# Performance work log

Measured on AMD Instinct MI355X. Metric: run time of the kernel, lower is better.

Reference implementation:

```python
import jax, jax.numpy as jnp
import numpy as np

NEGATIVE_RATIO = 3.0


def setup_inputs() -> dict:
    key = jax.random.key(0)
    k1, k2, k3, k4, k5 = jax.random.split(key, 5)
    B, N, C = 64, 8732, 81  # batch, num_priors (SSD300), num_classes (COCO)
    pred_conf = jax.random.normal(k1, (B, N, C), dtype=jnp.float32)
    pred_loc = jax.random.normal(k2, (B, N, 4), dtype=jnp.float32)
    labels = jax.random.randint(k3, (B, N), 1, C)
    is_pos = jax.random.uniform(k4, (B, N)) < 0.03
    labels = jnp.where(is_pos, labels, 0)
    labels = labels.at[:, 0].set(1)  # guarantee >=1 positive per image
    gt_conf = jax.nn.one_hot(labels, C, dtype=jnp.float32)
    pos = (labels > 0)[..., None].astype(jnp.float32)
    gt_loc = jax.random.normal(k5, (B, N, 4), dtype=jnp.float32) * pos
    return {"pred_conf": pred_conf, "pred_loc": pred_loc,
            "gt_conf": gt_conf, "gt_loc": gt_loc}


def reference(pred_conf, pred_loc, gt_conf, gt_loc):
    B, N, _ = pred_conf.shape
    # ----- conf loss: cross entropy against one-hot gt -----
    conf_loss = -(jax.nn.log_softmax(pred_conf, axis=-1) * gt_conf).sum(-1)  # [B, N]
    pos_mask = gt_conf[:, :, 0] == 0  # non-background priors
    num_pos = pos_mask.sum(-1).astype(pred_conf.dtype)  # [B]
    pos_conf_loss = jnp.where(pos_mask, conf_loss, 0.0).sum(-1)  # [B]
    # ----- hard negative mining: keep losses strictly above k-th largest negative loss -----
    num_neg = num_pos * NEGATIVE_RATIO  # [B], float
    neg_loss = jnp.where(pos_mask, 0.0, conf_loss)  # zero out positives
    sorted_desc = -jnp.sort(-neg_loss, axis=-1)  # descending per row
    k = jnp.clip(num_neg.astype(jnp.int32), 0, N - 1)  # [B]
    thresh = jnp.take_along_axis(sorted_desc, k[:, None], axis=-1)  # [B, 1]
    neg_mask = neg_loss > thresh  # only true on negatives (pos entries are 0)
    neg_conf_loss = jnp.where(neg_mask, conf_loss, 0.0).sum(-1)  # [B]
    conf_total = pos_conf_loss / num_pos + neg_conf_loss / num_neg  # [B]
    # ----- loc loss: smooth L1 on priors with nonzero gt_loc -----
    loc_mask = gt_loc != 0  # [B, N, 4]
    num_pos_loc = jnp.any(loc_mask, axis=-1).sum(-1).astype(pred_loc.dtype)  # [B]
    diff = jnp.abs(pred_loc - gt_loc)
    smooth_l1 = jnp.where(diff < 1.0, 0.5 * diff * diff, diff - 0.5)
    loc_total = jnp.where(loc_mask, smooth_l1, 0.0).sum((-1, -2)) / num_pos_loc  # [B]
    return (conf_total + loc_total).mean()
```

## Files before the change

### kernel.cpp

```cpp
#include <hip/hip_runtime.h>
#include <math.h>

#define BB 64
#define NN 8732
#define CC 81
#define TR 64
#define TPB 4
#define CBX ((NN + TR * TPB - 1) / (TR * TPB))
#define LBX 5

__global__ void init_kernel(unsigned* acc, float* out) {
    int i = threadIdx.x;
    if (i < 4 * BB) acc[i] = 0u;
    if (i == 0) out[0] = 0.f;
}

__device__ __forceinline__ float4 ld4g(const float* __restrict__ p, size_t gf, size_t TOTF) {
    if (gf + 4 <= TOTF) return *(const float4*)(p + gf);
    float4 r; float* rp = (float*)&r;
    #pragma unroll
    for (int c = 0; c < 4; ++c) rp[c] = (gf + c < TOTF) ? p[gf + c] : 0.f;
    return r;
}

__global__ __launch_bounds__(256) void fused_kernel(
        const float* __restrict__ pred_conf,
        const float* __restrict__ gt_conf,
        const float* __restrict__ pred_loc,
        const float* __restrict__ gt_loc,
        float* __restrict__ neg_loss,
        int* __restrict__ num_pos,
        float* __restrict__ pos_sum,
        float* __restrict__ loc_cnt,
        float* __restrict__ loc_sum) {
    const int b   = blockIdx.y;
    const int tid = threadIdx.x;

    if (blockIdx.x >= CBX) {
        const int lb = blockIdx.x - CBX;
        const float4* pl = (const float4*)pred_loc;
        const float4* gl = (const float4*)gt_loc;
        float sum = 0.f, cnt = 0.f;
        #pragma unroll
        for (int j = 0; j < 8; ++j) {
            int n = lb * 2048 + j * 256 + tid;
            if (n < NN) {
                size_t idx = (size_t)b * NN + n;
                float4 p = pl[idx];
                float4 g = gl[idx];
                bool any = false;
                float pv[4] = {p.x, p.y, p.z, p.w};
                float gv[4] = {g.x, g.y, g.z, g.w};
                #pragma unroll
                for (int c = 0; c < 4; ++c) {
                    if (gv[c] != 0.f) {
                        any = true;
                        float d = fabsf(pv[c] - gv[c]);
                        sum += (d < 1.f) ? 0.5f * d * d : d - 0.5f;
                    }
                }
                if (any) cnt += 1.f;
            }
        }
        for (int o = 32; o; o >>= 1) {
            sum += __shfl_down(sum, o, 64);
            cnt += __shfl_down(cnt, o, 64);
        }
        __shared__ float ls_sum, ls_cnt;
        if (tid == 0) { ls_sum = 0.f; ls_cnt = 0.f; }
        __syncthreads();
        if ((tid & 63) == 0) { atomicAdd(&ls_sum, sum); atomicAdd(&ls_cnt, cnt); }
        __syncthreads();
        if (tid == 0) { atomicAdd(&loc_sum[b], ls_sum); atomicAdd(&loc_cnt[b], ls_cnt); }
        return;
    }

    __shared__ float lbuf[TR * CC + 8];
    __shared__ int   s_cnt;
    __shared__ float s_sum;
    float4* l4 = (float4*)lbuf;

    const size_t TOTF = (size_t)BB * NN * CC;
    const int tile0 = blockIdx.x * TPB;
    const int r = tid >> 2;
    const int h = tid & 3;

    if (tid == 0) { s_cnt = 0; s_sum = 0.f; }

    float4 rv[6];
    float  gt0p;
    int rowBn = tile0 * TR;
    int nrn   = min(TR, NN - rowBn);
    size_t a0n; int shn, t4n;
    {
        size_t seg = ((size_t)b * NN + rowBn) * CC;
        a0n = seg & ~(size_t)3; shn = (int)(seg - a0n);
        t4n = (shn + nrn * CC + 3) >> 2;
    }
    #pragma unroll
    for (int j = 0; j < 6; ++j) {
        int i = tid + 256 * j;
        if (i < t4n) rv[j] = ld4g(pred_conf, a0n + 4 * (size_t)i, TOTF);
    }
    gt0p = (r < nrn) ? gt_conf[((size_t)b * NN + rowBn + r) * CC] : 1.f;

    for (int t = 0; t < TPB; ++t) {
        const int   c_rowB = rowBn, c_nr = nrn, c_sh = shn, c_t4 = t4n;
        const float c_gt0  = gt0p;
        if (c_rowB >= NN) break;

        __syncthreads();
        #pragma unroll
        for (int j = 0; j < 6; ++j) {
            int i = tid + 256 * j;
            if (i < c_t4) l4[i] = rv[j];
        }
        __syncthreads();

        const int nrowB = (tile0 + t + 1) * TR;
        if (t + 1 < TPB && nrowB < NN) {
            rowBn = nrowB; nrn = min(TR, NN - nrowB);
            size_t seg = ((size_t)b * NN + nrowB) * CC;
            a0n = seg & ~(size_t)3; shn = (int)(seg - a0n);
            t4n = (shn + nrn * CC + 3) >> 2;
            #pragma unroll
            for (int j = 0; j < 6; ++j) {
                int i = tid + 256 * j;
                if (i < t4n) rv[j] = ld4g(pred_conf, a0n + 4 * (size_t)i, TOTF);
            }
            gt0p = (r < nrn) ? gt_conf[((size_t)b * NN + rowBn + r) * CC] : 1.f;
        } else {
            rowBn = NN;
        }

        if (r < c_nr) {
            const int c0 = h * 20 + (h > 0 ? 1 : 0);
            const int nc = (h == 0) ? 21 : 20;
            const float* row = lbuf + c_sh + r * CC;
            const size_t gbase = ((size_t)b * NN + c_rowB + r) * CC;

            float v[21];
            #pragma unroll
            for (int j = 0; j < 21; ++j)
                v[j] = (j < nc) ? row[c0 + j] : -1e30f;

            float m = v[0];
            #pragma unroll
            for (int j = 1; j < 21; ++j) m = fmaxf(m, v[j]);
            m = fmaxf(m, __shfl_xor(m, 1, 64));
            m = fmaxf(m, __shfl_xor(m, 2, 64));

            float e = 0.f;
            #pragma unroll
            for (int j = 0; j < 21; ++j) e += __expf(v[j] - m);
            e += __shfl_xor(e, 1, 64);
            e += __shfl_xor(e, 2, 64);

            const bool pos = (c_gt0 == 0.f);
            float x_sel = v[0];
            if (pos) {
                float d = 0.f;
                #pragma unroll
                for (int j = 0; j < 21; ++j)
                    if (j < nc) d += gt_conf[gbase + c0 + j] * v[j];
                d += __shfl_xor(d, 1, 64);
                d += __shfl_xor(d, 2, 64);
                x_sel = d;
            }

            const float loss = m + __logf(e) - x_sel;
            if (h == 0) {
                neg_loss[(size_t)b * NN + c_rowB + r] = pos ? 0.f : loss;
                if (pos) { atomicAdd(&s_cnt, 1); atomicAdd(&s_sum, loss); }
            }
        }
    }

    __syncthreads();
    if (tid == 0 && s_cnt) {
        atomicAdd(&num_pos[b], s_cnt);
        atomicAdd(&pos_sum[b], s_sum);
    }
}

__global__ __launch_bounds__(256) void select_kernel(
        const float* __restrict__ neg_loss,
        const int*   __restrict__ num_pos,
        const float* __restrict__ pos_sum,
        const float* __restrict__ loc_cnt,
        const float* __restrict__ loc_sum,
        float* __restrict__ out) {
    const int b    = blockIdx.x;
    const int tid  = threadIdx.x;
    const int lane = tid & 63;
    __shared__ unsigned vals[NN];
    __shared__ unsigned hist[256];
    __shared__ unsigned sh_prefix, sh_r;
    __shared__ float    s_part[4];

    #pragma unroll 4
    for (int i = tid; i < NN; i += 256)
        vals[i] = __float_as_uint(neg_loss[(size_t)b * NN + i]);

    const int np = num_pos[b];
    const int k  = min(3 * np, NN - 1);
    if (tid == 0) { sh_prefix = 0u; sh_r = (unsigned)k; }
    __syncthreads();

    unsigned prefix_mask = 0u;
    for (int p = 3; p >= 0; --p) {
        const unsigned pref = sh_prefix;
        const unsigned r    = sh_r;
        hist[tid] = 0u;
        __syncthreads();

        for (int i0 = 0; i0 < NN; i0 += 256) {
            const int i = i0 + tid;
            const bool act = (i < NN) && ((vals[i] & prefix_mask) == pref);
            const unsigned v   = act ? vals[i] : 0u;
            const unsigned bin = (v >> (8 * p)) & 255u;
            unsigned long long mm = __ballot(act);
            #pragma unroll
            for (int bit = 0; bit < 8; ++bit) {
                unsigned long long s = __ballot(act && ((bin >> bit) & 1u));
                mm &= ((bin >> bit) & 1u) ? s : ~s;
            }
            if (act && ((mm & ((1ull << lane) - 1ull)) == 0ull))
                atomicAdd(&hist[bin], (unsigned)__popcll(mm));
        }
        __syncthreads();

        if (tid < 64) {
            const unsigned h0 = hist[4 * tid + 0];
            const unsigned h1 = hist[4 * tid + 1];
            const unsigned h2 = hist[4 * tid + 2];
            const unsigned h3 = hist[4 * tid + 3];
            unsigned T = h0 + h1 + h2 + h3;
            #pragma unroll
            for (int off = 1; off < 64; off <<= 1) {
                unsigned t2 = __shfl_down(T, off, 64);
                if (tid + off < 64) T += t2;
            }
            unsigned Tn = __shfl_down(T, 1, 64);
            if (tid == 63) Tn = 0u;
            const unsigned S4 = Tn, S3 = S4 + h3, S2 = S3 + h2, S1 = S2 + h1, S0 = S1 + h0;
            int bin = -1; unsigned Slo = 0u;
            if      (S1 <= r && r < S0) { bin = 4 * tid + 0; Slo = S1; }
            else if (S2 <= r && r < S1) { bin = 4 * tid + 1; Slo = S2; }
            else if (S3 <= r && r < S2) { bin = 4 * tid + 2; Slo = S3; }
            else if (S4 <= r && r < S3) { bin = 4 * tid + 3; Slo = S4; }
            if (bin >= 0) {
                sh_r = r - Slo;
                sh_prefix = pref | ((unsigned)bin << (8 * p));
            }
        }
        __syncthreads();
        prefix_mask |= 0xFFu << (8 * p);
    }

    const float thresh = __uint_as_float(sh_prefix);
    float s = 0.f;
    #pragma unroll 4
    for (int i = tid; i < NN; i += 256) {
        float v = __uint_as_float(vals[i]);
        if (v > thresh) s += v;
    }
    for (int o = 32; o; o >>= 1) s += __shfl_down(s, o, 64);
    if (lane == 0) s_part[tid >> 6] = s;
    __syncthreads();
    if (tid == 0) {
        float neg_sum = s_part[0] + s_part[1] + s_part[2] + s_part[3];
        float npf = (float)np;
        float res = pos_sum[b] / npf + neg_sum / (3.0f * npf) + loc_sum[b] / loc_cnt[b];
        atomicAdd(out, res * (1.0f / BB));
    }
}

extern "C" void kernel_launch(void* const* d_in, const int* in_sizes, int n_in,
                              void* d_out, int out_size, void* d_ws, size_t ws_size,
                              hipStream_t stream) {
    const float* pred_conf = (const float*)d_in[0];
    const float* pred_loc  = (const float*)d_in[1];
    const float* gt_conf   = (const float*)d_in[2];
    const float* gt_loc    = (const float*)d_in[3];

    float* neg      = (float*)d_ws;
    int*   num_pos  = (int*)(neg + (size_t)BB * NN);
    float* pos_sum  = (float*)(num_pos + BB);
    float* loc_cnt  = pos_sum + BB;
    float* loc_sum  = loc_cnt + BB;

    init_kernel<<<1, 256, 0, stream>>>((unsigned*)num_pos, (float*)d_out);

    dim3 fgrid(CBX + LBX, BB);
    fused_kernel<<<fgrid, 256, 0, stream>>>(pred_conf, gt_conf, pred_loc, gt_loc,
                                            neg, num_pos, pos_sum, loc_cnt, loc_sum);

    select_kernel<<<BB, 256, 0, stream>>>(neg, num_pos, pos_sum, loc_cnt, loc_sum,
                                          (float*)d_out);
}
```

Baseline: 414.4 us.

## Give each wave its own LDS tile and drop block-wide barriers in conf loss

Restructures the cross-entropy stage so each 64-lane wave stages and processes its own 16-row tile in a private LDS region, removing the block-level __syncthreads between staging and compute. Positive-count and positive-loss accumulation moves from shared-memory atomics to per-lane registers reduced with wave shuffles, and the loc path now issues per-wave global atomics instead of a shared reduction. The intent is to cut barrier stalls and shared atomic contention, at the cost of smaller per-load tiles and more global atomics.

Measured after the change: 420.5 us. About the same (+1.5%).

```diff
diff --git a/kernel.cpp b/kernel.cpp
--- a/kernel.cpp
+++ b/kernel.cpp
@@ -4,10 +4,13 @@
 #define BB 64
 #define NN 8732
 #define CC 81
-#define TR 64
-#define TPB 4
-#define CBX ((NN + TR * TPB - 1) / (TR * TPB))
+#define TR2 16
+#define WIT 4
+#define WROWS (TR2 * WIT)
+#define BROWS (WROWS * 4)
+#define CBX ((NN + BROWS - 1) / BROWS)
 #define LBX 5
+#define LSEG4 328
 
 __global__ void init_kernel(unsigned* acc, float* out) {
     int i = threadIdx.x;
@@ -66,78 +69,78 @@
             sum += __shfl_down(sum, o, 64);
             cnt += __shfl_down(cnt, o, 64);
         }
-        __shared__ float ls_sum, ls_cnt;
-        if (tid == 0) { ls_sum = 0.f; ls_cnt = 0.f; }
-        __syncthreads();
-        if ((tid & 63) == 0) { atomicAdd(&ls_sum, sum); atomicAdd(&ls_cnt, cnt); }
-        __syncthreads();
-        if (tid == 0) { atomicAdd(&loc_sum[b], ls_sum); atomicAdd(&loc_cnt[b], ls_cnt); }
+        if ((tid & 63) == 0) {
+            atomicAdd(&loc_sum[b], sum);
+            atomicAdd(&loc_cnt[b], cnt);
+        }
         return;
     }
 
-    __shared__ float lbuf[TR * CC + 8];
-    __shared__ int   s_cnt;
-    __shared__ float s_sum;
-    float4* l4 = (float4*)lbuf;
+    __shared__ float4 lbuf4[4][LSEG4];
 
     const size_t TOTF = (size_t)BB * NN * CC;
-    const int tile0 = blockIdx.x * TPB;
-    const int r = tid >> 2;
-    const int h = tid & 3;
-
-    if (tid == 0) { s_cnt = 0; s_sum = 0.f; }
+    const int wave = tid >> 6;
+    const int lane = tid & 63;
+    const int q    = lane >> 2;
+    const int h    = lane & 3;
+    float*  lws = (float*)lbuf4[wave];
+    float4* l4  = lbuf4[wave];
+
+    const int rowB0 = blockIdx.x * BROWS + wave * WROWS;
+
+    int   my_cnt = 0;
+    float my_sum = 0.f;
 
     float4 rv[6];
-    float  gt0p;
-    int rowBn = tile0 * TR;
-    int nrn   = min(TR, NN - rowBn);
-    size_t a0n; int shn, t4n;
-    {
-        size_t seg = ((size_t)b * NN + rowBn) * CC;
-        a0n = seg & ~(size_t)3; shn = (int)(seg - a0n);
-        t4n = (shn + nrn * CC + 3) >> 2;
-    }
-    #pragma unroll
-    for (int j = 0; j < 6; ++j) {
-        int i = tid + 256 * j;
-        if (i < t4n) rv[j] = ld4g(pred_conf, a0n + 4 * (size_t)i, TOTF);
-    }
-    gt0p = (r < nrn) ? gt_conf[((size_t)b * NN + rowBn + r) * CC] : 1.f;
-
-    for (int t = 0; t < TPB; ++t) {
-        const int   c_rowB = rowBn, c_nr = nrn, c_sh = shn, c_t4 = t4n;
-        const float c_gt0  = gt0p;
-        if (c_rowB >= NN) break;
-
-        __syncthreads();
+    float  gt0p = 1.f;
+    int curB  = rowB0;
+    int curNr = min(TR2, NN - curB);
+    int curSh = 0, curT4 = 0;
+    if (curNr > 0) {
+        size_t seg = ((size_t)b * NN + curB) * CC;
+        size_t a0  = seg & ~(size_t)3;
+        curSh = (int)(seg - a0);
+        curT4 = (curSh + curNr * CC + 3) >> 2;
         #pragma unroll
         for (int j = 0; j < 6; ++j) {
-            int i = tid + 256 * j;
+            int i = lane + 64 * j;
+            if (i < curT4) rv[j] = ld4g(pred_conf, a0 + 4 * (size_t)i, TOTF);
+        }
+        if (q < curNr) gt0p = gt_conf[((size_t)b * NN + curB + q) * CC];
+    }
+
+    for (int it = 0; it < WIT; ++it) {
+        const int   c_rowB = curB, c_nr = curNr, c_sh = curSh, c_t4 = curT4;
+        const float c_gt0  = gt0p;
+        if (c_nr <= 0) break;
+
+        #pragma unroll
+        for (int j = 0; j < 6; ++j) {
+            int i = lane + 64 * j;
             if (i < c_t4) l4[i] = rv[j];
         }
-        __syncthreads();
-
-        const int nrowB = (tile0 + t + 1) * TR;
-        if (t + 1 < TPB && nrowB < NN) {
-            rowBn = nrowB; nrn = min(TR, NN - nrowB);
-            size_t seg = ((size_t)b * NN + nrowB) * CC;
-            a0n = seg & ~(size_t)3; shn = (int)(seg - a0n);
-            t4n = (shn + nrn * CC + 3) >> 2;
+
+        const int nB  = rowB0 + (it + 1) * TR2;
+        const int nNr = (it + 1 < WIT) ? min(TR2, NN - nB) : 0;
+        if (nNr > 0) {
+            size_t seg = ((size_t)b * NN + nB) * CC;
+            size_t a0  = seg & ~(size_t)3;
+            curSh = (int)(seg - a0);
+            curT4 = (curSh + nNr * CC + 3) >> 2;
             #pragma unroll
             for (int j = 0; j < 6; ++j) {
-                int i = tid + 256 * j;
-                if (i < t4n) rv[j] = ld4g(pred_conf, a0n + 4 * (size_t)i, TOTF);
-            }
-            gt0p = (r < nrn) ? gt_conf[((size_t)b * NN + rowBn + r) * CC] : 1.f;
-        } else {
-            rowBn = NN;
-        }
-
-        if (r < c_nr) {
+                int i = lane + 64 * j;
+                if (i < curT4) rv[j] = ld4g(pred_conf, a0 + 4 * (size_t)i, TOTF);
+            }
+            gt0p = (q < nNr) ? gt_conf[((size_t)b * NN + nB + q) * CC] : 1.f;
+        }
+        curB = nB; curNr = nNr;
+
+        if (q < c_nr) {
             const int c0 = h * 20 + (h > 0 ? 1 : 0);
             const int nc = (h == 0) ? 21 : 20;
-            const float* row = lbuf + c_sh + r * CC;
-            const size_t gbase = ((size_t)b * NN + c_rowB + r) * CC;
+            const float* row = lws + c_sh + q * CC;
+            const size_t gbase = ((size_t)b * NN + c_rowB + q) * CC;
 
             float v[21];
             #pragma unroll
@@ -170,16 +173,20 @@
 
             const float loss = m + __logf(e) - x_sel;
             if (h == 0) {
-                neg_loss[(size_t)b * NN + c_rowB + r] = pos ? 0.f : loss;
-                if (pos) { atomicAdd(&s_cnt, 1); atomicAdd(&s_sum, loss); }
-            }
-        }
-    }
-
-    __syncthreads();
-    if (tid == 0 && s_cnt) {
-        atomicAdd(&num_pos[b], s_cnt);
-        atomicAdd(&pos_sum[b], s_sum);
+                neg_loss[(size_t)b * NN + c_rowB + q] = pos ? 0.f : loss;
+                if (pos) { my_cnt++; my_sum += loss; }
+            }
+        }
+    }
+
+    #pragma unroll
+    for (int off = 4; off < 64; off <<= 1) {
+        my_sum += __shfl_down(my_sum, off, 64);
+        my_cnt += __shfl_down(my_cnt, off, 64);
+    }
+    if (lane == 0 && my_cnt) {
+        atomicAdd(&num_pos[b], my_cnt);
+        atomicAdd(&pos_sum[b], my_sum);
     }
 }
 
```
